# Performance work log

Measured on AMD Instinct MI355X. Metric: run time of the kernel, lower is better.

The kernel has to match this reference:

```python
import jax, jax.numpy as jnp
import numpy as np

HID = 5120
H = 40
DN = 128   # qk_nope_head_dim
DR = 64    # qk_rope_head_dim
DQK = DN + DR
DV = 128   # v_head_dim
QLR = 1536 # q_lora_rank
KVLR = 512 # kv_lora_rank
EPS = 1e-6
ROPE_THETA = 10000.0


def setup_inputs() -> dict:
    key = jax.random.key(0)
    ks = jax.random.split(key, 8)
    B, S = 2, 2048
    s = 0.02
    return {
        "x": jax.random.normal(ks[0], (B, S, HID), dtype=jnp.float32),
        # fused down-projection: q_lora + kv_lora + k_pe
        "w_a": jax.random.normal(ks[1], (HID, QLR + KVLR + DR), dtype=jnp.float32) * s,
        "q_ln_w": jnp.ones((QLR,), dtype=jnp.float32),
        "kv_ln_w": jnp.ones((KVLR,), dtype=jnp.float32),
        "w_qb": jax.random.normal(ks[2], (QLR, H * DQK), dtype=jnp.float32) * s,
        "w_kvb": jax.random.normal(ks[3], (KVLR, H * (DN + DV)), dtype=jnp.float32) * s,
        "w_o": jax.random.normal(ks[4], (H * DV, HID), dtype=jnp.float32) * s,
    }


def _rmsnorm(x, w):
    var = jnp.mean(jnp.square(x), axis=-1, keepdims=True)
    return x * jax.lax.rsqrt(var + EPS) * w


def _rope_cos_sin(S, dtype):
    half = DR // 2
    inv_freq = 1.0 / (ROPE_THETA ** (jnp.arange(half, dtype=jnp.float32) / half))
    ang = jnp.arange(S, dtype=jnp.float32)[:, None] * inv_freq[None, :]  # [S, half]
    return jnp.cos(ang).astype(dtype), jnp.sin(ang).astype(dtype)


def _apply_rope(t, cos, sin):
    # t: [..., S, h, DR]; cos/sin: [S, DR/2]
    t1, t2 = jnp.split(t, 2, axis=-1)
    c = cos[None, :, None, :]
    s = sin[None, :, None, :]
    return jnp.concatenate([t1 * c - t2 * s, t2 * c + t1 * s], axis=-1)


def mla_forward(x, w_a, q_ln_w, kv_ln_w, w_qb, w_kvb, w_o):
    B, S, _ = x.shape
    # fused low-rank down-projection
    a = x @ w_a  # [B, S, QLR + KVLR + DR]
    q_c = _rmsnorm(a[..., :QLR], q_ln_w)
    kv_c = _rmsnorm(a[..., QLR:QLR + KVLR], kv_ln_w)
    k_pe = a[..., QLR + KVLR:]  # [B, S, DR] shared across heads (MQA-style)

    q = (q_c @ w_qb).reshape(B, S, H, DQK)
    q_nope, q_pe = q[..., :DN], q[..., DN:]
    kv = (kv_c @ w_kvb).reshape(B, S, H, DN + DV)
    k_nope, v = kv[..., :DN], kv[..., DN:]

    cos, sin = _rope_cos_sin(S, x.dtype)
    q_pe = _apply_rope(q_pe, cos, sin)                  # [B,S,H,DR]
    k_pe = _apply_rope(k_pe[:, :, None, :], cos, sin)    # [B,S,1,DR]

    qh = jnp.concatenate([q_nope, q_pe], axis=-1)                                 # [B,S,H,DQK]
    kh = jnp.concatenate([k_nope, jnp.broadcast_to(k_pe, (B, S, H, DR))], axis=-1)  # [B,S,H,DQK]

    scale = 1.0 / np.sqrt(DQK)
    scores = jnp.einsum('bqhd,bkhd->bhqk', qh, kh) * scale
    causal = jnp.tril(jnp.ones((S, S), dtype=bool))
    scores = jnp.where(causal[None, None], scores, jnp.finfo(scores.dtype).min)
    attn = jax.nn.softmax(scores, axis=-1)
    o = jnp.einsum('bhqk,bkhd->bqhd', attn, v).reshape(B, S, H * DV)
    return o @ w_o


def reference(x, w_a, q_ln_w, kv_ln_w, w_qb, w_kvb, w_o):
    return mla_forward(x, w_a, q_ln_w, kv_ln_w, w_qb, w_kvb, w_o)
```

## Files before the change

kernel.cpp:

```cpp
#include <hip/hip_runtime.h>

typedef unsigned short u16;
typedef __attribute__((ext_vector_type(8))) short bf16x8;
typedef __attribute__((ext_vector_type(4))) float f32x4;

__device__ __forceinline__ float bf2f(u16 u) {
  unsigned int x = ((unsigned int)u) << 16;
  return __builtin_bit_cast(float, x);
}
__device__ __forceinline__ u16 f2bf(float f) {
  unsigned int x = __builtin_bit_cast(unsigned int, f);
  x += 0x7fff + ((x >> 16) & 1);
  return (u16)(x >> 16);
}
__device__ __forceinline__ void gload16(const u16* g, u16* l) {
  __builtin_amdgcn_global_load_lds((const __attribute__((address_space(1))) void*)g,
                                   (__attribute__((address_space(3))) void*)l, 16, 0, 0);
}
#define MFMA16(a, b, c) __builtin_amdgcn_mfma_f32_16x16x32_bf16(a, b, c, 0, 0, 0)

__global__ __launch_bounds__(256) void convert_k(const float* __restrict__ in,
                                                 u16* __restrict__ out, int n4) {
  const int i = blockIdx.x * 256 + threadIdx.x;
  if (i < n4) {
    float4 f = ((const float4*)in)[i];
    ushort4 v;
    v.x = f2bf(f.x); v.y = f2bf(f.y); v.z = f2bf(f.z); v.w = f2bf(f.w);
    ((ushort4*)out)[i] = v;
  }
}

__global__ __launch_bounds__(256) void transpose_k(const float* __restrict__ in,
                                                   u16* __restrict__ out,
                                                   int R, int C) {
  __shared__ u16 t[64][65];
  const int r0 = blockIdx.x * 64, c0 = blockIdx.y * 64;
  const int x = threadIdx.x & 15, y = threadIdx.x >> 4;
  if (c0 < C) {
#pragma unroll
    for (int i = 0; i < 4; i++) {
      const float* g = in + (size_t)(r0 + y + 16 * i) * C + c0 + 4 * x;
      float4 v = *(const float4*)g;
      t[y + 16 * i][4 * x + 0] = f2bf(v.x);
      t[y + 16 * i][4 * x + 1] = f2bf(v.y);
      t[y + 16 * i][4 * x + 2] = f2bf(v.z);
      t[y + 16 * i][4 * x + 3] = f2bf(v.w);
    }
    __syncthreads();
#pragma unroll
    for (int i = 0; i < 4; i++) {
      const int cc = y + 16 * i;
      ushort4 v;
      v.x = t[4 * x + 0][cc];
      v.y = t[4 * x + 1][cc];
      v.z = t[4 * x + 2][cc];
      v.w = t[4 * x + 3][cc];
      *(ushort4*)(out + (size_t)(c0 + cc) * R + r0 + 4 * x) = v;
    }
  } else {
    ushort4 z = {0, 0, 0, 0};
#pragma unroll
    for (int i = 0; i < 4; i++)
      *(ushort4*)(out + (size_t)(c0 + y + 16 * i) * R + r0 + 4 * x) = z;
  }
}

template <int MODE>
__global__ __launch_bounds__(256) void gemm_bt(const u16* __restrict__ A, int lda,
                                               const u16* __restrict__ Bt, int ldb,
                                               void* __restrict__ Cp, int ldc,
                                               u16* __restrict__ C1, int K) {
  __shared__ u16 lA[128 * 32];
  __shared__ u16 lB[128 * 32];
  const int tid = threadIdx.x;
  const int m0 = blockIdx.x * 128, n0 = blockIdx.y * 128;
  const int w = tid >> 6, lane = tid & 63, r = lane & 15, quad = lane >> 4;
  const int wr = (w >> 1) * 64, wc = (w & 1) * 64;

  f32x4 acc[4][4];
#pragma unroll
  for (int i = 0; i < 4; i++)
#pragma unroll
    for (int j = 0; j < 4; j++) acc[i][j] = (f32x4){0.f, 0.f, 0.f, 0.f};

  const int r_a = tid >> 2;
  const int c_a = (tid & 3) * 8;
  const u16* gA = A + (size_t)(m0 + r_a) * lda + c_a;
  const u16* gB = Bt + (size_t)(n0 + r_a) * ldb + c_a;
  u16* lAb = lA + (tid & 192) * 8;
  u16* lBb = lB + (tid & 192) * 8;

  for (int k0 = 0; k0 < K; k0 += 32) {
    __syncthreads();
    gload16(gA + k0, lAb);
    gload16(gA + (size_t)64 * lda + k0, lAb + 2048);
    gload16(gB + k0, lBb);
    gload16(gB + (size_t)64 * ldb + k0, lBb + 2048);
    __syncthreads();
    bf16x8 af[4], bf[4];
#pragma unroll
    for (int i = 0; i < 4; i++) af[i] = *(const bf16x8*)&lA[(wr + i * 16 + r) * 32 + quad * 8];
#pragma unroll
    for (int j = 0; j < 4; j++) bf[j] = *(const bf16x8*)&lB[(wc + j * 16 + r) * 32 + quad * 8];
#pragma unroll
    for (int i = 0; i < 4; i++)
#pragma unroll
      for (int j = 0; j < 4; j++) acc[i][j] = MFMA16(af[i], bf[j], acc[i][j]);
  }

#pragma unroll
  for (int i = 0; i < 4; i++) {
#pragma unroll
    for (int j = 0; j < 4; j++) {
#pragma unroll
      for (int reg = 0; reg < 4; reg++) {
        const int row = m0 + wr + i * 16 + quad * 4 + reg;
        const int col = n0 + wc + j * 16 + r;
        const float fv = acc[i][j][reg];
        if (MODE == 0) {
          ((u16*)Cp)[(size_t)row * ldc + col] = f2bf(fv);
        } else if (MODE == 2) {
          ((float*)Cp)[(size_t)row * ldc + col] = fv;
        } else {
          const int hh = col >> 8, cc = col & 255;
          if (cc < 128) {
            ((u16*)Cp)[(size_t)row * 5120 + hh * 128 + cc] = f2bf(fv);
          } else {
            const int bb = row >> 11, ss = row & 2047;
            C1[(((size_t)(bb * 40 + hh)) * 128 + (cc - 128)) * 2048 + ss] = f2bf(fv);
          }
        }
      }
    }
  }
}

__global__ __launch_bounds__(256) void rmsnorm_k(u16* __restrict__ a,
                                                 const float* __restrict__ qw,
                                                 const float* __restrict__ kvw) {
  const int row = blockIdx.x, seg = blockIdx.y;
  const int off = seg ? 1536 : 0;
  const int width = seg ? 512 : 1536;
  const float* wp = seg ? kvw : qw;
  u16* p = a + (size_t)row * 2176 + off;
  const int tid = threadIdx.x;
  float ss = 0.f;
  for (int i = tid; i < width; i += 256) {
    float v = bf2f(p[i]);
    ss += v * v;
  }
#pragma unroll
  for (int o = 32; o >= 1; o >>= 1) ss += __shfl_xor(ss, o, 64);
  __shared__ float red[4];
  if ((tid & 63) == 0) red[tid >> 6] = ss;
  __syncthreads();
  const float tot = red[0] + red[1] + red[2] + red[3];
  const float rs = rsqrtf(tot / (float)width + 1e-6f);
  for (int i = tid; i < width; i += 256) p[i] = f2bf(bf2f(p[i]) * rs * wp[i]);
}

__global__ __launch_bounds__(256) void rope_k(u16* __restrict__ a, u16* __restrict__ q) {
  const int row = blockIdx.x;
  const int s = row & 2047;
  const int tid = threadIdx.x;
  __shared__ float cs[32], sn[32];
  if (tid < 32) {
    float inv = powf(10000.f, -(float)tid * (1.f / 32.f));
    float ang = (float)s * inv;
    cs[tid] = cosf(ang);
    sn[tid] = sinf(ang);
  }
  __syncthreads();
  if (tid < 32) {
    u16* p = a + (size_t)row * 2176 + 2048;
    float t1 = bf2f(p[tid]), t2 = bf2f(p[tid + 32]);
    p[tid] = f2bf(t1 * cs[tid] - t2 * sn[tid]);
    p[tid + 32] = f2bf(t2 * cs[tid] + t1 * sn[tid]);
  }
  for (int item = tid; item < 1280; item += 256) {
    const int hh = item >> 5, i = item & 31;
    u16* p = q + (size_t)row * 7680 + hh * 192 + 128;
    float t1 = bf2f(p[i]), t2 = bf2f(p[i + 32]);
    p[i] = f2bf(t1 * cs[i] - t2 * sn[i]);
    p[i + 32] = f2bf(t2 * cs[i] + t1 * sn[i]);
  }
}

__global__ __launch_bounds__(256) void attn_k(const u16* __restrict__ q,
                                              const u16* __restrict__ kn,
                                              const u16* __restrict__ aB,
                                              const u16* __restrict__ vT,
                                              u16* __restrict__ o) {
  __shared__ u16 lK[2][6 * 32 * 32];
  __shared__ u16 lV[2][128 * 32];
  __shared__ u16 lP[4][16 * 36];
  const int hwid = blockIdx.x;
  const int lid = (hwid & 7) * 320 + (hwid >> 3);
  const int qt = 31 - (lid & 31);
  const int h = (lid >> 5) % 40;
  const int b = lid / 1280;
  const int q0 = qt * 64;
  const int tid = threadIdx.x, w = tid >> 6, lane = tid & 63, r = lane & 15, quad = lane >> 4;
  const int srow = lane >> 2, sseg = (lane & 3) * 8;

  bf16x8 qf[6];
  {
    const u16* qrow = q + (((size_t)(b * 2048 + q0 + w * 16 + r)) * 40 + h) * 192;
#pragma unroll
    for (int kd = 0; kd < 6; kd++) qf[kd] = *(const bf16x8*)(qrow + kd * 32 + quad * 8);
  }
  f32x4 oa[8];
#pragma unroll
  for (int f = 0; f < 8; f++) oa[f] = (f32x4){0.f, 0.f, 0.f, 0.f};
  float m_i[4], l_i[4];
#pragma unroll
  for (int t = 0; t < 4; t++) {
    m_i[t] = -3.0e38f;
    l_i[t] = 0.f;
  }
  u16* lPw = lP[w];
  const int nkt = 2 * (qt + 1);

  auto stage = [&](int bufi, int kt) {
    const int k0 = kt * 32;
    u16* lKb = lK[bufi];
    u16* lVb = lV[bufi];
#pragma unroll
    for (int c = w; c < 12; c += 4) {
      const int kd = c >> 1;
      const int row = (c & 1) * 16 + srow;
      const u16* g =
          (kd < 4)
              ? kn + (((size_t)(b * 2048 + k0 + row)) * 40 + h) * 128 + kd * 32 + sseg
              : aB + ((size_t)(b * 2048 + k0 + row)) * 2176 + 2048 + (kd - 4) * 32 + sseg;
      gload16(g, lKb + c * 512 + lane * 8);
    }
#pragma unroll
    for (int c = w; c < 8; c += 4) {
      const int row = c * 16 + srow;
      const u16* g = vT + (((size_t)(b * 40 + h)) * 128 + row) * 2048 + k0 + sseg;
      gload16(g, lVb + c * 512 + lane * 8);
    }
  };

  stage(0, 0);

  for (int kt = 0; kt < nkt; kt++) {
    const int k0 = kt * 32;
    if (kt + 1 < nkt) {
      stage((kt + 1) & 1, kt + 1);
      asm volatile("s_waitcnt vmcnt(5)" ::: "memory");
    } else {
      asm volatile("s_waitcnt vmcnt(0)" ::: "memory");
    }
    __builtin_amdgcn_s_barrier();
    __builtin_amdgcn_sched_barrier(0);
    const u16* lKb = lK[kt & 1];
    const u16* lVb = lV[kt & 1];
    if (k0 <= q0 + w * 16 + 15) {
      f32x4 s[2];
      s[0] = (f32x4){0.f, 0.f, 0.f, 0.f};
      s[1] = (f32x4){0.f, 0.f, 0.f, 0.f};
      __builtin_amdgcn_s_setprio(1);
#pragma unroll
      for (int kd = 0; kd < 6; kd++) {
#pragma unroll
        for (int j = 0; j < 2; j++) {
          bf16x8 bk = *(const bf16x8*)&lKb[kd * 1024 + (j * 16 + r) * 32 + quad * 8];
          s[j] = MFMA16(qf[kd], bk, s[j]);
        }
      }
      __builtin_amdgcn_s_setprio(0);
      const float sc = 0.0721687836487032f;
      const bool diag = (k0 + 31 > q0 + w * 16);
      const int kq = k0 + r - q0 - w * 16 - quad * 4;
      float mc[4];
#pragma unroll
      for (int t = 0; t < 4; t++) {
        float mx = -3.0e38f;
#pragma unroll
        for (int j = 0; j < 2; j++) {
          float v = s[j][t] * sc;
          if (diag && (kq + j * 16 > t)) v = -3.0e38f;
          s[j][t] = v;
          mx = fmaxf(mx, v);
        }
        mc[t] = mx;
      }
#pragma unroll
      for (int off = 1; off < 16; off <<= 1) {
#pragma unroll
        for (int t = 0; t < 4; t++) mc[t] = fmaxf(mc[t], __shfl_xor(mc[t], off, 64));
      }
      bool grow = false;
#pragma unroll
      for (int t = 0; t < 4; t++) grow = grow || (mc[t] > m_i[t]);
      if (__any(grow)) {
#pragma unroll
        for (int t = 0; t < 4; t++) {
          const float mn = fmaxf(m_i[t], mc[t]);
          const float al = __expf(m_i[t] - mn);
          m_i[t] = mn;
          l_i[t] *= al;
#pragma unroll
          for (int f = 0; f < 8; f++) oa[f][t] *= al;
        }
      }
      float ls[4];
#pragma unroll
      for (int t = 0; t < 4; t++) {
        float sum = 0.f;
#pragma unroll
        for (int j = 0; j < 2; j++) {
          float pv = __expf(s[j][t] - m_i[t]);
          s[j][t] = pv;
          sum += pv;
        }
        ls[t] = sum;
      }
#pragma unroll
      for (int off = 1; off < 16; off <<= 1) {
#pragma unroll
        for (int t = 0; t < 4; t++) ls[t] += __shfl_xor(ls[t], off, 64);
      }
#pragma unroll
      for (int t = 0; t < 4; t++) l_i[t] += ls[t];
#pragma unroll
      for (int t = 0; t < 4; t++) {
#pragma unroll
        for (int j = 0; j < 2; j++)
          lPw[(quad * 4 + t) * 36 + j * 16 + r] = f2bf(s[j][t]);
      }
      bf16x8 ap = *(const bf16x8*)&lPw[r * 36 + quad * 8];
      __builtin_amdgcn_s_setprio(1);
#pragma unroll
      for (int f = 0; f < 8; f++) {
        bf16x8 bv = *(const bf16x8*)&lVb[(f * 16 + r) * 32 + quad * 8];
        oa[f] = MFMA16(ap, bv, oa[f]);
      }
      __builtin_amdgcn_s_setprio(0);
    }
    asm volatile("s_waitcnt lgkmcnt(0)" ::: "memory");
    __builtin_amdgcn_s_barrier();
  }
#pragma unroll
  for (int t = 0; t < 4; t++) {
    const float inv = 1.0f / l_i[t];
    u16* op = o + ((size_t)(b * 2048 + q0 + w * 16 + quad * 4 + t)) * 5120 + h * 128;
#pragma unroll
    for (int f = 0; f < 8; f++) op[f * 16 + r] = f2bf(oa[f][t] * inv);
  }
}

extern "C" void kernel_launch(void* const* d_in, const int* in_sizes, int n_in,
                              void* d_out, int out_size, void* d_ws, size_t ws_size,
                              hipStream_t stream) {
  const float* x = (const float*)d_in[0];
  const float* w_a = (const float*)d_in[1];
  const float* qlw = (const float*)d_in[2];
  const float* kvlw = (const float*)d_in[3];
  const float* w_qb = (const float*)d_in[4];
  const float* w_kvb = (const float*)d_in[5];
  const float* w_o = (const float*)d_in[6];
  float* out = (float*)d_out;

  char* base = (char*)d_ws;
  u16* aB   = (u16*)(base);
  u16* qB   = (u16*)(base + 17825792ULL);
  u16* knop = (u16*)(base + 80740352ULL);
  u16* vT   = (u16*)(base + 122683392ULL);
  u16* xB   = (u16*)(base + 164626432ULL);
  u16* waT  = (u16*)(base + 206569472ULL);
  u16* wqbT = (u16*)(base + 164626432ULL);
  u16* wkvT = (u16*)(base + 164626432ULL);
  u16* woT  = (u16*)(base + 164626432ULL);
  u16* oB   = (u16*)(base + 217055232ULL);

  convert_k<<<20480, 256, 0, stream>>>(x, xB, 5242880);
  transpose_k<<<dim3(5120 / 64, 2176 / 64), 256, 0, stream>>>(w_a, waT, 5120, 2112);
  gemm_bt<0><<<dim3(32, 17), 256, 0, stream>>>(xB, 5120, waT, 5120, aB, 2176, nullptr, 5120);
  rmsnorm_k<<<dim3(4096, 2), 256, 0, stream>>>(aB, qlw, kvlw);
  transpose_k<<<dim3(1536 / 64, 7680 / 64), 256, 0, stream>>>(w_qb, wqbT, 1536, 7680);
  gemm_bt<0><<<dim3(32, 60), 256, 0, stream>>>(aB, 2176, wqbT, 1536, qB, 7680, nullptr, 1536);
  transpose_k<<<dim3(512 / 64, 10240 / 64), 256, 0, stream>>>(w_kvb, wkvT, 512, 10240);
  gemm_bt<1><<<dim3(32, 80), 256, 0, stream>>>(aB + 1536, 2176, wkvT, 512, knop, 0, vT, 512);
  transpose_k<<<dim3(5120 / 64, 5120 / 64), 256, 0, stream>>>(w_o, woT, 5120, 5120);
  rope_k<<<4096, 256, 0, stream>>>(aB, qB);
  attn_k<<<2560, 256, 0, stream>>>(qB, knop, aB, vT, oB);
  gemm_bt<2><<<dim3(32, 40), 256, 0, stream>>>(oB, 5120, woT, 5120, out, 5120, nullptr, 5120);
}
```

Measured before the change: 1.421 ms.

## Load V fragments directly to registers and compute row sums via MFMA

V tiles are no longer staged through shared memory. Each lane loads its V fragments straight into registers with global_load_dwordx4, and the vmcnt waits are reworked to overlap these loads with the QK and softmax work. The softmax row sum is obtained by an extra MFMA against a ones vector, which removes the shuffle reduction. Exponentials now use exp2 with a folded scale, and P is packed with a single cvt_pk_bf16. The aim is to cut LDS traffic and VALU or shuffle work, at the cost of more VGPRs and uncoalesced per-lane global loads of V.

After: 1.477 ms. 4.0% more time.

```diff
diff --git a/kernel.cpp b/kernel.cpp
--- a/kernel.cpp
+++ b/kernel.cpp
@@ -3,6 +3,7 @@
 typedef unsigned short u16;
 typedef __attribute__((ext_vector_type(8))) short bf16x8;
 typedef __attribute__((ext_vector_type(4))) float f32x4;
+typedef __attribute__((ext_vector_type(4))) unsigned int u32x4;
 
 __device__ __forceinline__ float bf2f(u16 u) {
   unsigned int x = ((unsigned int)u) << 16;
@@ -13,9 +14,23 @@
   x += 0x7fff + ((x >> 16) & 1);
   return (u16)(x >> 16);
 }
+__device__ __forceinline__ float exp2f_fast(float x) {
+  return __builtin_amdgcn_exp2f(x);
+}
 __device__ __forceinline__ void gload16(const u16* g, u16* l) {
   __builtin_amdgcn_global_load_lds((const __attribute__((address_space(1))) void*)g,
                                    (__attribute__((address_space(3))) void*)l, 16, 0, 0);
+}
+__device__ __forceinline__ bf16x8 gload_v(const u16* sbase, unsigned voff_bytes) {
+  u32x4 r;
+  asm volatile("global_load_dwordx4 %0, %1, %2"
+               : "=v"(r) : "v"(voff_bytes), "s"(sbase) : "memory");
+  return __builtin_bit_cast(bf16x8, r);
+}
+__device__ __forceinline__ unsigned cvt_pk_bf16(float lo, float hi) {
+  unsigned r;
+  asm("v_cvt_pk_bf16_f32 %0, %1, %2" : "=v"(r) : "v"(lo), "v"(hi));
+  return r;
 }
 #define MFMA16(a, b, c) __builtin_amdgcn_mfma_f32_16x16x32_bf16(a, b, c, 0, 0, 0)
 
@@ -192,7 +207,6 @@
                                               const u16* __restrict__ vT,
                                               u16* __restrict__ o) {
   __shared__ u16 lK[2][6 * 32 * 32];
-  __shared__ u16 lV[2][128 * 32];
   __shared__ u16 lP[4][16 * 36];
   const int hwid = blockIdx.x;
   const int lid = (hwid & 7) * 320 + (hwid >> 3);
@@ -209,22 +223,24 @@
 #pragma unroll
     for (int kd = 0; kd < 6; kd++) qf[kd] = *(const bf16x8*)(qrow + kd * 32 + quad * 8);
   }
-  f32x4 oa[8];
+  f32x4 oa[8], oL;
 #pragma unroll
   for (int f = 0; f < 8; f++) oa[f] = (f32x4){0.f, 0.f, 0.f, 0.f};
-  float m_i[4], l_i[4];
-#pragma unroll
-  for (int t = 0; t < 4; t++) {
-    m_i[t] = -3.0e38f;
-    l_i[t] = 0.f;
-  }
+  oL = (f32x4){0.f, 0.f, 0.f, 0.f};
+  float m_i[4];
+#pragma unroll
+  for (int t = 0; t < 4; t++) m_i[t] = -3.0e38f;
+  bf16x8 ones;
+#pragma unroll
+  for (int e = 0; e < 8; e++) ones[e] = (short)0x3F80;
   u16* lPw = lP[w];
   const int nkt = 2 * (qt + 1);
+  const unsigned voff0 =
+      (((unsigned)((b * 40 + h) * 128 + r)) * 2048 + (unsigned)(quad * 8)) * 2u;
 
   auto stage = [&](int bufi, int kt) {
     const int k0 = kt * 32;
     u16* lKb = lK[bufi];
-    u16* lVb = lV[bufi];
 #pragma unroll
     for (int c = w; c < 12; c += 4) {
       const int kd = c >> 1;
@@ -235,29 +251,30 @@
               : aB + ((size_t)(b * 2048 + k0 + row)) * 2176 + 2048 + (kd - 4) * 32 + sseg;
       gload16(g, lKb + c * 512 + lane * 8);
     }
-#pragma unroll
-    for (int c = w; c < 8; c += 4) {
-      const int row = c * 16 + srow;
-      const u16* g = vT + (((size_t)(b * 40 + h)) * 128 + row) * 2048 + k0 + sseg;
-      gload16(g, lVb + c * 512 + lane * 8);
-    }
   };
 
   stage(0, 0);
 
   for (int kt = 0; kt < nkt; kt++) {
     const int k0 = kt * 32;
+    bf16x8 vf[8];
+    {
+      const unsigned vk = voff0 + (unsigned)(k0 * 2);
+#pragma unroll
+      for (int f = 0; f < 8; f++) vf[f] = gload_v(vT, vk + (unsigned)(f * 65536));
+    }
     if (kt + 1 < nkt) {
       stage((kt + 1) & 1, kt + 1);
-      asm volatile("s_waitcnt vmcnt(5)" ::: "memory");
+      asm volatile("s_waitcnt vmcnt(11)" ::: "memory");
     } else {
-      asm volatile("s_waitcnt vmcnt(0)" ::: "memory");
+      asm volatile("s_waitcnt vmcnt(8)" ::: "memory");
     }
     __builtin_amdgcn_s_barrier();
     __builtin_amdgcn_sched_barrier(0);
     const u16* lKb = lK[kt & 1];
-    const u16* lVb = lV[kt & 1];
-    if (k0 <= q0 + w * 16 + 15) {
+    const bool active = (k0 <= q0 + w * 16 + 15);
+    bf16x8 ap;
+    if (active) {
       f32x4 s[2];
       s[0] = (f32x4){0.f, 0.f, 0.f, 0.f};
       s[1] = (f32x4){0.f, 0.f, 0.f, 0.f};
@@ -271,7 +288,7 @@
         }
       }
       __builtin_amdgcn_s_setprio(0);
-      const float sc = 0.0721687836487032f;
+      const float SCL2 = 0.10411754f;
       const bool diag = (k0 + 31 > q0 + w * 16);
       const int kq = k0 + r - q0 - w * 16 - quad * 4;
       float mc[4];
@@ -280,7 +297,7 @@
         float mx = -3.0e38f;
 #pragma unroll
         for (int j = 0; j < 2; j++) {
-          float v = s[j][t] * sc;
+          float v = s[j][t];
           if (diag && (kq + j * 16 > t)) v = -3.0e38f;
           s[j][t] = v;
           mx = fmaxf(mx, v);
@@ -299,53 +316,43 @@
 #pragma unroll
         for (int t = 0; t < 4; t++) {
           const float mn = fmaxf(m_i[t], mc[t]);
-          const float al = __expf(m_i[t] - mn);
+          const float al = exp2f_fast((m_i[t] - mn) * SCL2);
           m_i[t] = mn;
-          l_i[t] *= al;
+          oL[t] *= al;
 #pragma unroll
           for (int f = 0; f < 8; f++) oa[f][t] *= al;
         }
       }
-      float ls[4];
 #pragma unroll
       for (int t = 0; t < 4; t++) {
-        float sum = 0.f;
-#pragma unroll
-        for (int j = 0; j < 2; j++) {
-          float pv = __expf(s[j][t] - m_i[t]);
-          s[j][t] = pv;
-          sum += pv;
-        }
-        ls[t] = sum;
-      }
-#pragma unroll
-      for (int off = 1; off < 16; off <<= 1) {
-#pragma unroll
-        for (int t = 0; t < 4; t++) ls[t] += __shfl_xor(ls[t], off, 64);
-      }
-#pragma unroll
-      for (int t = 0; t < 4; t++) l_i[t] += ls[t];
-#pragma unroll
-      for (int t = 0; t < 4; t++) {
-#pragma unroll
-        for (int j = 0; j < 2; j++)
-          lPw[(quad * 4 + t) * 36 + j * 16 + r] = f2bf(s[j][t]);
-      }
-      bf16x8 ap = *(const bf16x8*)&lPw[r * 36 + quad * 8];
+        const float p0 = exp2f_fast((s[0][t] - m_i[t]) * SCL2);
+        const float p1 = exp2f_fast((s[1][t] - m_i[t]) * SCL2);
+        const unsigned pk = cvt_pk_bf16(p0, p1);
+        lPw[(quad * 4 + t) * 36 + r] = (u16)pk;
+        lPw[(quad * 4 + t) * 36 + 16 + r] = (u16)(pk >> 16);
+      }
+      ap = *(const bf16x8*)&lPw[r * 36 + quad * 8];
+    }
+    if (kt + 1 < nkt) {
+      asm volatile("s_waitcnt vmcnt(3)" ::: "memory");
+    } else {
+      asm volatile("s_waitcnt vmcnt(0)" ::: "memory");
+    }
+    __builtin_amdgcn_sched_barrier(0);
+    if (active) {
       __builtin_amdgcn_s_setprio(1);
 #pragma unroll
-      for (int f = 0; f < 8; f++) {
-        bf16x8 bv = *(const bf16x8*)&lVb[(f * 16 + r) * 32 + quad * 8];
-        oa[f] = MFMA16(ap, bv, oa[f]);
-      }
+      for (int f = 0; f < 8; f++) oa[f] = MFMA16(ap, vf[f], oa[f]);
+      oL = MFMA16(ap, ones, oL);
       __builtin_amdgcn_s_setprio(0);
     }
     asm volatile("s_waitcnt lgkmcnt(0)" ::: "memory");
     __builtin_amdgcn_s_barrier();
   }
+  asm volatile("s_waitcnt vmcnt(0)" ::: "memory");
 #pragma unroll
   for (int t = 0; t < 4; t++) {
-    const float inv = 1.0f / l_i[t];
+    const float inv = 1.0f / oL[t];
     u16* op = o + ((size_t)(b * 2048 + q0 + w * 16 + quad * 4 + t)) * 5120 + h * 128;
 #pragma unroll
     for (int f = 0; f < 8; f++) op[f * 16 + r] = f2bf(oa[f][t] * inv);
```

## Transpose QK scores to cut softmax shuffles and compute row sums via MFMA

Applied to the files above, without the earlier changes.

The QK^T MFMA operands are swapped so each lane holds one query row's scores. The row max then needs only two cross-quad shuffles instead of a 16-lane butterfly. Exponentials use exp2 with the scale folded into the log2 factor, P is packed to bf16 with v_cvt_pk_bf16 and written in 64-bit stores, and the row-sum reduction is replaced by an extra MFMA against a ones vector. The rescale factor now needs per-row shuffles to broadcast back to output layout, and the row sums are taken from bf16-rounded probabilities.

Result: faster. 1.327 ms (-6.6%).

```diff
diff --git a/kernel.cpp b/kernel.cpp
--- a/kernel.cpp
+++ b/kernel.cpp
@@ -1,6 +1,7 @@
 #include <hip/hip_runtime.h>
 
 typedef unsigned short u16;
+typedef unsigned long long u64;
 typedef __attribute__((ext_vector_type(8))) short bf16x8;
 typedef __attribute__((ext_vector_type(4))) float f32x4;
 
@@ -13,9 +14,17 @@
   x += 0x7fff + ((x >> 16) & 1);
   return (u16)(x >> 16);
 }
+__device__ __forceinline__ float exp2f_fast(float x) {
+  return __builtin_amdgcn_exp2f(x);
+}
 __device__ __forceinline__ void gload16(const u16* g, u16* l) {
   __builtin_amdgcn_global_load_lds((const __attribute__((address_space(1))) void*)g,
                                    (__attribute__((address_space(3))) void*)l, 16, 0, 0);
+}
+__device__ __forceinline__ unsigned cvt_pk_bf16(float lo, float hi) {
+  unsigned r;
+  asm("v_cvt_pk_bf16_f32 %0, %1, %2" : "=v"(r) : "v"(lo), "v"(hi));
+  return r;
 }
 #define MFMA16(a, b, c) __builtin_amdgcn_mfma_f32_16x16x32_bf16(a, b, c, 0, 0, 0)
 
@@ -193,7 +202,7 @@
                                               u16* __restrict__ o) {
   __shared__ u16 lK[2][6 * 32 * 32];
   __shared__ u16 lV[2][128 * 32];
-  __shared__ u16 lP[4][16 * 36];
+  __shared__ u16 lP[4][16 * 40];
   const int hwid = blockIdx.x;
   const int lid = (hwid & 7) * 320 + (hwid >> 3);
   const int qt = 31 - (lid & 31);
@@ -209,15 +218,14 @@
 #pragma unroll
     for (int kd = 0; kd < 6; kd++) qf[kd] = *(const bf16x8*)(qrow + kd * 32 + quad * 8);
   }
-  f32x4 oa[8];
+  f32x4 oa[8], oL;
 #pragma unroll
   for (int f = 0; f < 8; f++) oa[f] = (f32x4){0.f, 0.f, 0.f, 0.f};
-  float m_i[4], l_i[4];
-#pragma unroll
-  for (int t = 0; t < 4; t++) {
-    m_i[t] = -3.0e38f;
-    l_i[t] = 0.f;
-  }
+  oL = (f32x4){0.f, 0.f, 0.f, 0.f};
+  float m_i = -3.0e38f;
+  bf16x8 ones;
+#pragma unroll
+  for (int e = 0; e < 8; e++) ones[e] = (short)0x3F80;
   u16* lPw = lP[w];
   const int nkt = 2 * (qt + 1);
 
@@ -237,8 +245,7 @@
     }
 #pragma unroll
     for (int c = w; c < 8; c += 4) {
-      const int row = c * 16 + srow;
-      const u16* g = vT + (((size_t)(b * 40 + h)) * 128 + row) * 2048 + k0 + sseg;
+      const u16* g = vT + (((size_t)(b * 40 + h)) * 128 + c * 16 + srow) * 2048 + k0 + sseg;
       gload16(g, lVb + c * 512 + lane * 8);
     }
   };
@@ -267,77 +274,54 @@
 #pragma unroll
         for (int j = 0; j < 2; j++) {
           bf16x8 bk = *(const bf16x8*)&lKb[kd * 1024 + (j * 16 + r) * 32 + quad * 8];
-          s[j] = MFMA16(qf[kd], bk, s[j]);
+          s[j] = MFMA16(bk, qf[kd], s[j]);
         }
       }
       __builtin_amdgcn_s_setprio(0);
-      const float sc = 0.0721687836487032f;
+      const float SCL2 = 0.10411754f;
       const bool diag = (k0 + 31 > q0 + w * 16);
-      const int kq = k0 + r - q0 - w * 16 - quad * 4;
-      float mc[4];
-#pragma unroll
-      for (int t = 0; t < 4; t++) {
-        float mx = -3.0e38f;
-#pragma unroll
-        for (int j = 0; j < 2; j++) {
-          float v = s[j][t] * sc;
-          if (diag && (kq + j * 16 > t)) v = -3.0e38f;
+      const int dlt = q0 + w * 16 + r - k0 - quad * 4;
+      float mx = -3.0e38f;
+#pragma unroll
+      for (int j = 0; j < 2; j++) {
+#pragma unroll
+        for (int t = 0; t < 4; t++) {
+          float v = s[j][t];
+          if (diag && (j * 16 + t > dlt)) v = -3.0e38f;
           s[j][t] = v;
           mx = fmaxf(mx, v);
         }
-        mc[t] = mx;
-      }
-#pragma unroll
-      for (int off = 1; off < 16; off <<= 1) {
-#pragma unroll
-        for (int t = 0; t < 4; t++) mc[t] = fmaxf(mc[t], __shfl_xor(mc[t], off, 64));
-      }
-      bool grow = false;
-#pragma unroll
-      for (int t = 0; t < 4; t++) grow = grow || (mc[t] > m_i[t]);
-      if (__any(grow)) {
+      }
+      mx = fmaxf(mx, __shfl_xor(mx, 16, 64));
+      mx = fmaxf(mx, __shfl_xor(mx, 32, 64));
+      if (__any(mx > m_i)) {
+        const float mn = fmaxf(m_i, mx);
+        const float al = exp2f_fast((m_i - mn) * SCL2);
+        m_i = mn;
 #pragma unroll
         for (int t = 0; t < 4; t++) {
-          const float mn = fmaxf(m_i[t], mc[t]);
-          const float al = __expf(m_i[t] - mn);
-          m_i[t] = mn;
-          l_i[t] *= al;
-#pragma unroll
-          for (int f = 0; f < 8; f++) oa[f][t] *= al;
+          const float alb = __shfl(al, quad * 4 + t, 64);
+          oL[t] *= alb;
+#pragma unroll
+          for (int f = 0; f < 8; f++) oa[f][t] *= alb;
         }
       }
-      float ls[4];
-#pragma unroll
-      for (int t = 0; t < 4; t++) {
-        float sum = 0.f;
-#pragma unroll
-        for (int j = 0; j < 2; j++) {
-          float pv = __expf(s[j][t] - m_i[t]);
-          s[j][t] = pv;
-          sum += pv;
-        }
-        ls[t] = sum;
-      }
-#pragma unroll
-      for (int off = 1; off < 16; off <<= 1) {
-#pragma unroll
-        for (int t = 0; t < 4; t++) ls[t] += __shfl_xor(ls[t], off, 64);
-      }
-#pragma unroll
-      for (int t = 0; t < 4; t++) l_i[t] += ls[t];
-#pragma unroll
-      for (int t = 0; t < 4; t++) {
-#pragma unroll
-        for (int j = 0; j < 2; j++)
-          lPw[(quad * 4 + t) * 36 + j * 16 + r] = f2bf(s[j][t]);
-      }
-      bf16x8 ap = *(const bf16x8*)&lPw[r * 36 + quad * 8];
+#pragma unroll
+      for (int j = 0; j < 2; j++) {
+        const unsigned lo = cvt_pk_bf16(exp2f_fast((s[j][0] - m_i) * SCL2),
+                                        exp2f_fast((s[j][1] - m_i) * SCL2));
+        const unsigned hi = cvt_pk_bf16(exp2f_fast((s[j][2] - m_i) * SCL2),
+                                        exp2f_fast((s[j][3] - m_i) * SCL2));
+        *(u64*)&lPw[r * 40 + j * 16 + quad * 4] = ((u64)hi << 32) | lo;
+      }
+      bf16x8 ap = *(const bf16x8*)&lPw[r * 40 + quad * 8];
       __builtin_amdgcn_s_setprio(1);
 #pragma unroll
       for (int f = 0; f < 8; f++) {
         bf16x8 bv = *(const bf16x8*)&lVb[(f * 16 + r) * 32 + quad * 8];
         oa[f] = MFMA16(ap, bv, oa[f]);
       }
+      oL = MFMA16(ap, ones, oL);
       __builtin_amdgcn_s_setprio(0);
     }
     asm volatile("s_waitcnt lgkmcnt(0)" ::: "memory");
@@ -345,7 +329,7 @@
   }
 #pragma unroll
   for (int t = 0; t < 4; t++) {
-    const float inv = 1.0f / l_i[t];
+    const float inv = 1.0f / oL[t];
     u16* op = o + ((size_t)(b * 2048 + q0 + w * 16 + quad * 4 + t)) * 5120 + h * 128;
 #pragma unroll
     for (int f = 0; f < 8; f++) op[f * 16 + r] = f2bf(oa[f][t] * inv);
```
